# Kernel tuning notes

Hardware: AMD Instinct MI355X
Metric: run time of the kernel (lower is better)

The kernel has to match this reference:

```python
import jax, jax.numpy as jnp
import numpy as np

MIN_NORM = 1e-7

def _norm(x):
    return jnp.maximum(jnp.sqrt(jnp.sum(x * x, axis=-1, keepdims=True)), MIN_NORM)

def _artanh(x):
    return jnp.arctanh(jnp.clip(x, -1.0 + 1e-6, 1.0 - 1e-6))

def tan_k(x, k):
    sq = jnp.sqrt(-k)
    return jnp.tanh(sq * x) / sq

def artan_k(x, k):
    sq = jnp.sqrt(-k)
    return _artanh(sq * x) / sq

def mobius_add(x, y, k):
    xy = jnp.sum(x * y, axis=-1, keepdims=True)
    x2 = jnp.sum(x * x, axis=-1, keepdims=True)
    y2 = jnp.sum(y * y, axis=-1, keepdims=True)
    num = (1.0 - 2.0 * k * xy - k * y2) * x + (1.0 + k * x2) * y
    den = 1.0 - 2.0 * k * xy + (k * k) * x2 * y2
    return num / jnp.maximum(den, MIN_NORM)

def expmap0(u, k):
    un = _norm(u)
    return tan_k(un, k) * u / un

def logmap0(y, k):
    yn = _norm(y)
    return artan_k(yn, k) * y / yn

def mobius_matvec(M, x, k):
    mx = x @ M.T
    xn = _norm(x)
    mxn = _norm(mx)
    return tan_k(mxn / xn * artan_k(xn, k), k) * mx / mxn

def mobius_pmul(w, x, k):
    wx = w * x
    xn = _norm(x)
    wxn = _norm(wx)
    return tan_k(wxn / xn * artan_k(xn, k), k) * wx / wxn

def setup_inputs() -> dict:
    B, S, D_IN, H = 64, 128, 768, 768
    key = jax.random.key(0)
    ks = jax.random.split(key, 5)
    stdv = 1.0 / np.sqrt(H)
    # inputs scaled small so points lie well inside the Poincare ball
    inputs = jax.random.normal(ks[0], (B, S, D_IN), dtype=jnp.float32) * 1e-3
    timestamps = jax.random.uniform(ks[1], (B, S), dtype=jnp.float32)
    h0 = jnp.zeros((B, H), dtype=jnp.float32)
    c0 = jnp.zeros((B, H), dtype=jnp.float32)
    W_all = jax.random.uniform(ks[2], (H, 4 * H), minval=-stdv, maxval=stdv, dtype=jnp.float32)
    U_all = jax.random.uniform(ks[3], (4 * H, D_IN), minval=-stdv, maxval=stdv, dtype=jnp.float32)
    W_d = jax.random.uniform(ks[4], (H, H), minval=-stdv, maxval=stdv, dtype=jnp.float32)
    c = jnp.float32(-1.0)  # Poincare ball curvature
    return {"inputs": inputs, "timestamps": timestamps, "h0": h0, "c0": c0,
            "W_all": W_all, "U_all": U_all, "W_d": W_d, "c": c}

def reference(inputs, timestamps, h0, c0, W_all, U_all, W_d, c):
    k = c
    W_f, W_i, W_o, W_ct = jnp.split(W_all, 4, axis=1)
    U_f, U_i, U_o, U_ct = jnp.split(U_all, 4, axis=0)

    def one_rnn_transform(W, h, U, x):
        return mobius_add(mobius_matvec(W, h, k), mobius_matvec(U, x, k), k)

    def step(carry, xs):
        h, cc = carry
        x, t = xs  # x: (B, D_in), t: (B,)
        c_s1 = expmap0(jnp.tanh(logmap0(mobius_matvec(W_d, cc, k), k)), k)
        t_exp = jnp.broadcast_to(t[:, None], c_s1.shape)
        c_s2 = mobius_pmul(c_s1, t_exp, k)
        c_l = mobius_add(-c_s1, cc, k)
        c_adj = mobius_add(c_l, c_s2, k)
        f = jax.nn.sigmoid(logmap0(one_rnn_transform(W_f, h, U_f, x), k))
        i = jax.nn.sigmoid(logmap0(one_rnn_transform(W_i, h, U_i, x), k))
        o = jax.nn.sigmoid(logmap0(one_rnn_transform(W_o, h, U_o, x), k))
        c_tmp = jax.nn.sigmoid(logmap0(one_rnn_transform(W_ct, h, U_ct, x), k))
        new_c = mobius_add(mobius_pmul(i, c_tmp, k), mobius_pmul(f, c_adj, k), k)
        new_h = mobius_pmul(o, expmap0(jnp.tanh(new_c), k), k)
        return (new_h, new_c), o

    xs = (inputs.transpose(1, 0, 2), timestamps.T)  # seq-major for scan
    (h_last, c_last), outs = jax.lax.scan(step, (h0, c0), xs)
    outputs = outs.transpose(1, 0, 2)  # (B, S, H)
    return (outputs, h_last, c_last)
```

## Files before the change

kernel.cpp:

```cpp
#include <hip/hip_runtime.h>
#include <hip/hip_bf16.h>
#include <math.h>

#define MINN 1e-7f

#define BB 64
#define SS 128
#define NCOL 3840

typedef float f4 __attribute__((ext_vector_type(4)));
typedef short bf16x8 __attribute__((ext_vector_type(8)));
typedef float f32x4 __attribute__((ext_vector_type(4)));

__device__ __forceinline__ float artanh_c(float x) {
  x = fminf(fmaxf(x, -1.0f + 1e-6f), 1.0f - 1e-6f);
  return atanhf(x);
}
__device__ __forceinline__ float tan_k_(float x, float sq) { return tanhf(sq * x) / sq; }
__device__ __forceinline__ float artan_k_(float x, float sq) { return artanh_c(sq * x) / sq; }

template <int N>
__device__ __forceinline__ void block_reduce_sum(float* v, float* red) {
#pragma unroll
  for (int m = 1; m < 64; m <<= 1) {
#pragma unroll
    for (int i = 0; i < N; ++i) v[i] += __shfl_xor(v[i], m, 64);
  }
  int wid = threadIdx.x >> 6;
  int lane = threadIdx.x & 63;
  if (lane == 0) {
#pragma unroll
    for (int i = 0; i < N; ++i) red[wid * N + i] = v[i];
  }
  __syncthreads();
#pragma unroll
  for (int i = 0; i < N; ++i) v[i] = red[i] + red[N + i] + red[2 * N + i] + red[3 * N + i];
  __syncthreads();
}

__global__ __launch_bounds__(256) void k_build_cw(const float* __restrict__ W_all,
                                                  const float* __restrict__ W_d,
                                                  __hip_bfloat16* __restrict__ CWh,
                                                  __hip_bfloat16* __restrict__ CWl) {
  int col = blockIdx.x;
#pragma unroll
  for (int p = 0; p < 3; ++p) {
    int k = threadIdx.x + 256 * p;
    float v;
    if (col < 768) {
      v = W_d[col * 768 + k];
    } else {
      int jm = col - 768;
      int g = jm / 768;
      int j2 = jm - g * 768;
      v = W_all[j2 * 3072 + g * 768 + k];
    }
    __hip_bfloat16 h = __float2bfloat16(v);
    CWh[(size_t)col * 768 + k] = h;
    CWl[(size_t)col * 768 + k] = __float2bfloat16(v - __bfloat162float(h));
  }
}

__global__ __launch_bounds__(256) void k_init_state(
    const float* __restrict__ h0, const float* __restrict__ c0,
    float* __restrict__ ccR, float* __restrict__ hR,
    __hip_bfloat16* __restrict__ CH, __hip_bfloat16* __restrict__ CL,
    __hip_bfloat16* __restrict__ HH, __hip_bfloat16* __restrict__ HL) {
  int r = blockIdx.x;
#pragma unroll
  for (int p = 0; p < 3; ++p) {
    int j = threadIdx.x + 256 * p;
    float cv = c0[r * 768 + j];
    float hv = h0[r * 768 + j];
    ccR[r * 768 + j] = cv;
    hR[r * 768 + j] = hv;
    __hip_bfloat16 ch = __float2bfloat16(cv);
    CH[r * 768 + j] = ch;
    CL[r * 768 + j] = __float2bfloat16(cv - __bfloat162float(ch));
    __hip_bfloat16 hh = __float2bfloat16(hv);
    HH[r * 768 + j] = hh;
    HL[r * 768 + j] = __float2bfloat16(hv - __bfloat162float(hh));
  }
}

__global__ __launch_bounds__(256) void k_xnorm(const float* __restrict__ X,
                                               float* __restrict__ XN) {
  __shared__ float red[4];
  int r = blockIdx.x;
  float s = 0.f;
#pragma unroll
  for (int p = 0; p < 3; ++p) {
    float v = X[(size_t)r * 768 + threadIdx.x + 256 * p];
    s += v * v;
  }
#pragma unroll
  for (int m = 1; m < 64; m <<= 1) s += __shfl_xor(s, m, 64);
  if ((threadIdx.x & 63) == 0) red[threadIdx.x >> 6] = s;
  __syncthreads();
  if (threadIdx.x == 0) XN[r] = fmaxf(sqrtf(red[0] + red[1] + red[2] + red[3]), MINN);
}

__global__ __launch_bounds__(256) void k_split(const float* __restrict__ src,
                                               __hip_bfloat16* __restrict__ hi,
                                               __hip_bfloat16* __restrict__ lo, int n4) {
  int i = blockIdx.x * 256 + threadIdx.x;
  if (i >= n4) return;
  f4 v = *(const f4*)(src + (size_t)i * 4);
#pragma unroll
  for (int j = 0; j < 4; ++j) {
    float x = (j == 0) ? v.x : (j == 1) ? v.y : (j == 2) ? v.z : v.w;
    __hip_bfloat16 h = __float2bfloat16(x);
    float r = x - __bfloat162float(h);
    hi[(size_t)i * 4 + j] = h;
    lo[(size_t)i * 4 + j] = __float2bfloat16(r);
  }
}

__global__ __launch_bounds__(256) void k_gemm_xu_mfma(
    const __hip_bfloat16* __restrict__ Xh, const __hip_bfloat16* __restrict__ Xl,
    const __hip_bfloat16* __restrict__ Uh, const __hip_bfloat16* __restrict__ Ul,
    __hip_bfloat16* __restrict__ OUT) {
  int tid = threadIdx.x;
  int wave = tid >> 6, lane = tid & 63;
  int r = lane & 15, kg = lane >> 4;
  int i0 = blockIdx.x * 64 + wave * 16;
  int m0 = blockIdx.y * 64;
  const __hip_bfloat16* xh = Xh + (size_t)(i0 + r) * 768 + kg * 8;
  const __hip_bfloat16* xl = Xl + (size_t)(i0 + r) * 768 + kg * 8;
  const __hip_bfloat16* uh = Uh + (size_t)(m0 + r) * 768 + kg * 8;
  const __hip_bfloat16* ul = Ul + (size_t)(m0 + r) * 768 + kg * 8;
  f32x4 acc0 = {0.f, 0.f, 0.f, 0.f};
  f32x4 acc1 = acc0, acc2 = acc0, acc3 = acc0;
  for (int k0 = 0; k0 < 768; k0 += 32) {
    bf16x8 ah = *(const bf16x8*)(xh + k0);
    bf16x8 al = *(const bf16x8*)(xl + k0);
    bf16x8 b0h = *(const bf16x8*)(uh + k0);
    bf16x8 b0l = *(const bf16x8*)(ul + k0);
    bf16x8 b1h = *(const bf16x8*)(uh + 12288 + k0);
    bf16x8 b1l = *(const bf16x8*)(ul + 12288 + k0);
    bf16x8 b2h = *(const bf16x8*)(uh + 24576 + k0);
    bf16x8 b2l = *(const bf16x8*)(ul + 24576 + k0);
    bf16x8 b3h = *(const bf16x8*)(uh + 36864 + k0);
    bf16x8 b3l = *(const bf16x8*)(ul + 36864 + k0);
    acc0 = __builtin_amdgcn_mfma_f32_16x16x32_bf16(ah, b0h, acc0, 0, 0, 0);
    acc1 = __builtin_amdgcn_mfma_f32_16x16x32_bf16(ah, b1h, acc1, 0, 0, 0);
    acc2 = __builtin_amdgcn_mfma_f32_16x16x32_bf16(ah, b2h, acc2, 0, 0, 0);
    acc3 = __builtin_amdgcn_mfma_f32_16x16x32_bf16(ah, b3h, acc3, 0, 0, 0);
    acc0 = __builtin_amdgcn_mfma_f32_16x16x32_bf16(al, b0h, acc0, 0, 0, 0);
    acc1 = __builtin_amdgcn_mfma_f32_16x16x32_bf16(al, b1h, acc1, 0, 0, 0);
    acc2 = __builtin_amdgcn_mfma_f32_16x16x32_bf16(al, b2h, acc2, 0, 0, 0);
    acc3 = __builtin_amdgcn_mfma_f32_16x16x32_bf16(al, b3h, acc3, 0, 0, 0);
    acc0 = __builtin_amdgcn_mfma_f32_16x16x32_bf16(ah, b0l, acc0, 0, 0, 0);
    acc1 = __builtin_amdgcn_mfma_f32_16x16x32_bf16(ah, b1l, acc1, 0, 0, 0);
    acc2 = __builtin_amdgcn_mfma_f32_16x16x32_bf16(ah, b2l, acc2, 0, 0, 0);
    acc3 = __builtin_amdgcn_mfma_f32_16x16x32_bf16(ah, b3l, acc3, 0, 0, 0);
  }
#pragma unroll
  for (int j = 0; j < 4; ++j) {
    size_t row = (size_t)(i0 + kg * 4 + j) * 3072 + m0 + r;
    OUT[row] = __float2bfloat16(acc0[j]);
    OUT[row + 16] = __float2bfloat16(acc1[j]);
    OUT[row + 32] = __float2bfloat16(acc2[j]);
    OUT[row + 48] = __float2bfloat16(acc3[j]);
  }
}

__global__ __launch_bounds__(256) void k_step_gemm_mfma(
    const __hip_bfloat16* __restrict__ CWh, const __hip_bfloat16* __restrict__ CWl,
    const __hip_bfloat16* __restrict__ CH, const __hip_bfloat16* __restrict__ CL,
    const __hip_bfloat16* __restrict__ HH, const __hip_bfloat16* __restrict__ HL,
    float* __restrict__ GOUT) {
  int j = blockIdx.x;
  int wave = threadIdx.x >> 6, lane = threadIdx.x & 63;
  int r = lane & 15, kg = lane >> 4;
  int i0 = wave * 16;
  int m0 = j * 16;
  const __hip_bfloat16* sh = (j < 48 ? CH : HH) + (size_t)(i0 + r) * 768 + kg * 8;
  const __hip_bfloat16* sl = (j < 48 ? CL : HL) + (size_t)(i0 + r) * 768 + kg * 8;
  const __hip_bfloat16* wh = CWh + (size_t)(m0 + r) * 768 + kg * 8;
  const __hip_bfloat16* wl = CWl + (size_t)(m0 + r) * 768 + kg * 8;
  f32x4 acc = {0.f, 0.f, 0.f, 0.f};
#pragma unroll 4
  for (int k0 = 0; k0 < 768; k0 += 32) {
    bf16x8 ah = *(const bf16x8*)(sh + k0);
    bf16x8 al = *(const bf16x8*)(sl + k0);
    bf16x8 bh = *(const bf16x8*)(wh + k0);
    bf16x8 bl = *(const bf16x8*)(wl + k0);
    acc = __builtin_amdgcn_mfma_f32_16x16x32_bf16(ah, bh, acc, 0, 0, 0);
    acc = __builtin_amdgcn_mfma_f32_16x16x32_bf16(al, bh, acc, 0, 0, 0);
    acc = __builtin_amdgcn_mfma_f32_16x16x32_bf16(ah, bl, acc, 0, 0, 0);
  }
#pragma unroll
  for (int jj = 0; jj < 4; ++jj)
    GOUT[(size_t)(i0 + kg * 4 + jj) * NCOL + m0 + r] = acc[jj];
}

__global__ __launch_bounds__(256) void k_step_pw(
    const float* __restrict__ GOUT, const __hip_bfloat16* __restrict__ UG,
    const float* __restrict__ XN, const float* __restrict__ TS,
    const float* __restrict__ kptr, float* __restrict__ ccR, float* __restrict__ hR,
    __hip_bfloat16* __restrict__ CH, __hip_bfloat16* __restrict__ CL,
    __hip_bfloat16* __restrict__ HH, __hip_bfloat16* __restrict__ HL,
    float* __restrict__ out, int t) {
  __shared__ float red[64];
  int r = blockIdx.x;
  int tid = threadIdx.x;
  float kk = kptr[0];
  float sq = sqrtf(-kk);
  const float* grow = GOUT + r * NCOL;
  int i = r * SS + t;
  const __hip_bfloat16* urow = UG + (size_t)i * 3072;

  float cc[3], h[3], mv[3], gh[4][3], mx[4][3];
#pragma unroll
  for (int p = 0; p < 3; ++p) {
    int j = tid + 256 * p;
    cc[p] = ccR[r * 768 + j];
    h[p] = hR[r * 768 + j];
    mv[p] = grow[j];
#pragma unroll
    for (int g = 0; g < 4; ++g) {
      gh[g][p] = grow[768 + g * 768 + j];
      mx[g][p] = __bfloat162float(urow[g * 768 + j]);
    }
  }

  float sv[15];
#pragma unroll
  for (int q = 0; q < 15; ++q) sv[q] = 0.f;
#pragma unroll
  for (int p = 0; p < 3; ++p) {
    sv[0] += cc[p] * cc[p];
    sv[1] += h[p] * h[p];
    sv[2] += mv[p] * mv[p];
#pragma unroll
    for (int g = 0; g < 4; ++g) {
      sv[3 + g] += gh[g][p] * gh[g][p];
      sv[7 + g] += gh[g][p] * mx[g][p];
      sv[11 + g] += mx[g][p] * mx[g][p];
    }
  }
  block_reduce_sum<15>(sv, red);
  float c2 = sv[0], h2 = sv[1], mvn2 = sv[2];
  float xn_c = fmaxf(sqrtf(c2), MINN);
  float xn_h = fmaxf(sqrtf(h2), MINN);
  float mxn_d = fmaxf(sqrtf(mvn2), MINN);

  float r_d = (mxn_d / xn_c) * artan_k_(xn_c, sq);
  float twd = tan_k_(r_d, sq);
  float wdsc = twd / mxn_d;
  float yn_d = fmaxf(fabsf(twd), MINN);
  float lsc = (artan_k_(yn_d, sq) / yn_d) * wdsc;
  float th[3];
#pragma unroll
  for (int p = 0; p < 3; ++p) th[p] = tanhf(lsc * mv[p]);

  float uxn = XN[i];
  float ak_h = artan_k_(xn_h, sq);
  float ak_u = artan_k_(uxn, sq);
  float cAg[4], cBg[4], pscg[4];
#pragma unroll
  for (int g = 0; g < 4; ++g) {
    float ghn = fmaxf(sqrtf(sv[3 + g]), MINN);
    float tg = tan_k_((ghn / xn_h) * ak_h, sq);
    float wsc = tg / ghn;
    float w2 = tg * tg;
    float umxn = fmaxf(sqrtf(sv[11 + g]), MINN);
    float us = tan_k_((umxn / uxn) * ak_u, sq) / umxn;
    float u2 = us * us * sv[11 + g];
    float xy = wsc * us * sv[7 + g];
    float den = fmaxf(1.f - 2.f * kk * xy + kk * kk * w2 * u2, MINN);
    float a = (1.f - 2.f * kk * xy - kk * u2) / den;
    float b = (1.f + kk * w2) / den;
    float y2s = fmaxf(a * a * w2 + 2.f * a * b * xy + b * b * u2, 0.f);
    float yn = fmaxf(sqrtf(y2s), MINN);
    pscg[g] = artan_k_(yn, sq) / yn;
    cAg[g] = a * wsc;
    cBg[g] = b * us;
  }
  float gate[4][3];
#pragma unroll
  for (int g = 0; g < 4; ++g)
#pragma unroll
    for (int p = 0; p < 3; ++p)
      gate[g][p] = 1.f / (1.f + expf(-pscg[g] * (cAg[g] * gh[g][p] + cBg[g] * mx[g][p])));

  float s2v[2] = {0.f, 0.f};
#pragma unroll
  for (int p = 0; p < 3; ++p) {
    s2v[0] += th[p] * th[p];
    s2v[1] += th[p] * cc[p];
  }
  block_reduce_sum<2>(s2v, red);
  float un = fmaxf(sqrtf(s2v[0]), MINN);
  float esc = tan_k_(un, sq) / un;
  float cs1[3];
#pragma unroll
  for (int p = 0; p < 3; ++p) cs1[p] = esc * th[p];
  float d1 = esc * s2v[1];
  float s1sq = esc * esc * s2v[0];

  float tv = TS[r * SS + t];
  float xnt = fmaxf(sqrtf(768.f * tv * tv), MINN);
  float wxn_t = fmaxf(fabsf(tv) * sqrtf(s1sq), MINN);
  float s2s = tan_k_((wxn_t / xnt) * artan_k_(xnt, sq), sq) / wxn_t * tv;
  float s2sq = s2s * s2s * s1sq;

  float den_l = fmaxf(1.f + 2.f * kk * d1 + kk * kk * s1sq * c2, MINN);
  float al = (1.f + 2.f * kk * d1 - kk * c2) / den_l;
  float bl = (1.f + kk * s1sq) / den_l;
  float pcl = -al, qcl = bl;

  float xy2 = s2s * (pcl * s1sq + qcl * d1);
  float x2b = fmaxf(pcl * pcl * s1sq + 2.f * pcl * qcl * d1 + qcl * qcl * c2, 0.f);
  float y2b = s2sq;
  float den2 = fmaxf(1.f - 2.f * kk * xy2 + kk * kk * x2b * y2b, MINN);
  float a2 = (1.f - 2.f * kk * xy2 - kk * y2b) / den2;
  float b2 = (1.f + kk * x2b) / den2;
  float g1c = a2 * pcl + b2 * s2s;
  float g2c = a2 * qcl;
  float cadj[3];
#pragma unroll
  for (int p = 0; p < 3; ++p) cadj[p] = g1c * cs1[p] + g2c * cc[p];
  float adjsq = fmaxf(g1c * g1c * s1sq + 2.f * g1c * g2c * d1 + g2c * g2c * c2, 0.f);

  float wxi[3], wxf[3];
#pragma unroll
  for (int p = 0; p < 3; ++p) {
    wxi[p] = gate[1][p] * gate[3][p];
    wxf[p] = gate[0][p] * cadj[p];
  }
  float s3v[4] = {0.f, 0.f, 0.f, 0.f};
#pragma unroll
  for (int p = 0; p < 3; ++p) {
    s3v[0] += gate[3][p] * gate[3][p];
    s3v[1] += wxi[p] * wxi[p];
    s3v[2] += wxf[p] * wxf[p];
    s3v[3] += wxi[p] * wxf[p];
  }
  block_reduce_sum<4>(s3v, red);
  float xnct = fmaxf(sqrtf(s3v[0]), MINN);
  float wxni = fmaxf(sqrtf(s3v[1]), MINN);
  float psi = tan_k_((wxni / xnct) * artan_k_(xnct, sq), sq) / wxni;
  float pi2 = psi * psi * s3v[1];
  float xnadj = fmaxf(sqrtf(adjsq), MINN);
  float wxnf = fmaxf(sqrtf(s3v[2]), MINN);
  float psf = tan_k_((wxnf / xnadj) * artan_k_(xnadj, sq), sq) / wxnf;
  float pf2 = psf * psf * s3v[2];
  float xyp = psi * psf * s3v[3];
  float den3 = fmaxf(1.f - 2.f * kk * xyp + kk * kk * pi2 * pf2, MINN);
  float a3 = (1.f - 2.f * kk * xyp - kk * pf2) / den3;
  float b3 = (1.f + kk * pi2) / den3;
  float nc[3], tc[3];
#pragma unroll
  for (int p = 0; p < 3; ++p) {
    nc[p] = a3 * psi * wxi[p] + b3 * psf * wxf[p];
    tc[p] = tanhf(nc[p]);
  }
  float s4v[1] = {0.f};
#pragma unroll
  for (int p = 0; p < 3; ++p) s4v[0] += tc[p] * tc[p];
  block_reduce_sum<1>(s4v, red);
  float unh = fmaxf(sqrtf(s4v[0]), MINN);
  float ehs = tan_k_(unh, sq) / unh;
  float Esq = ehs * ehs * s4v[0];
  float En = fmaxf(sqrtf(Esq), MINN);
  float wxo[3];
#pragma unroll
  for (int p = 0; p < 3; ++p) wxo[p] = gate[2][p] * (ehs * tc[p]);
  float s5v[1] = {0.f};
#pragma unroll
  for (int p = 0; p < 3; ++p) s5v[0] += wxo[p] * wxo[p];
  block_reduce_sum<1>(s5v, red);
  float wxno = fmaxf(sqrtf(s5v[0]), MINN);
  float pso = tan_k_((wxno / En) * artan_k_(En, sq), sq) / wxno;

  size_t BSHc = (size_t)BB * SS * 768;
#pragma unroll
  for (int p = 0; p < 3; ++p) {
    int j = tid + 256 * p;
    out[((size_t)r * SS + t) * 768 + j] = gate[2][p];
    float ncv = nc[p];
    float nhv = pso * wxo[p];
    ccR[r * 768 + j] = ncv;
    hR[r * 768 + j] = nhv;
    __hip_bfloat16 chh = __float2bfloat16(ncv);
    CH[r * 768 + j] = chh;
    CL[r * 768 + j] = __float2bfloat16(ncv - __bfloat162float(chh));
    __hip_bfloat16 hhh = __float2bfloat16(nhv);
    HH[r * 768 + j] = hhh;
    HL[r * 768 + j] = __float2bfloat16(nhv - __bfloat162float(hhh));
    if (t == SS - 1) {
      out[BSHc + (size_t)r * 768 + j] = nhv;
      out[BSHc + (size_t)BB * 768 + (size_t)r * 768 + j] = ncv;
    }
  }
}

extern "C" void kernel_launch(void* const* d_in, const int* in_sizes, int n_in,
                              void* d_out, int out_size, void* d_ws, size_t ws_size,
                              hipStream_t stream) {
  const float* inputs = (const float*)d_in[0];
  const float* ts = (const float*)d_in[1];
  const float* h0 = (const float*)d_in[2];
  const float* c0 = (const float*)d_in[3];
  const float* W_all = (const float*)d_in[4];
  const float* U_all = (const float*)d_in[5];
  const float* W_d = (const float*)d_in[6];
  const float* kptr = (const float*)d_in[7];
  float* ws = (float*)d_ws;
  float* out = (float*)d_out;

  size_t oCWH = 0;
  size_t oCWL = oCWH + 1474560;
  size_t oCCR = oCWL + 1474560;
  size_t oHR = oCCR + 49152;
  size_t oCH = oHR + 49152;
  size_t oCL = oCH + 24576;
  size_t oHH = oCL + 24576;
  size_t oHL = oHH + 24576;
  size_t oGOUT = oHL + 24576;
  size_t oXN = oGOUT + (size_t)BB * NCOL;
  size_t oUG = oXN + 8192;
  size_t oXH = oUG + 12582912;
  size_t oXL = oXH + 3145728;
  size_t oUH = oXL + 3145728;
  size_t oUL = oUH + 1179648;

  __hip_bfloat16* cwh = (__hip_bfloat16*)(ws + oCWH);
  __hip_bfloat16* cwl = (__hip_bfloat16*)(ws + oCWL);
  float* ccr = ws + oCCR;
  float* hr = ws + oHR;
  __hip_bfloat16* ch = (__hip_bfloat16*)(ws + oCH);
  __hip_bfloat16* cl = (__hip_bfloat16*)(ws + oCL);
  __hip_bfloat16* hh = (__hip_bfloat16*)(ws + oHH);
  __hip_bfloat16* hl = (__hip_bfloat16*)(ws + oHL);
  float* gout = ws + oGOUT;
  float* xn = ws + oXN;
  __hip_bfloat16* ug = (__hip_bfloat16*)(ws + oUG);
  __hip_bfloat16* xhh = (__hip_bfloat16*)(ws + oXH);
  __hip_bfloat16* xll = (__hip_bfloat16*)(ws + oXL);
  __hip_bfloat16* uhh = (__hip_bfloat16*)(ws + oUH);
  __hip_bfloat16* ull = (__hip_bfloat16*)(ws + oUL);

  k_build_cw<<<NCOL, 256, 0, stream>>>(W_all, W_d, cwh, cwl);
  k_init_state<<<BB, 256, 0, stream>>>(h0, c0, ccr, hr, ch, cl, hh, hl);
  k_split<<<(6291456 / 4 + 255) / 256, 256, 0, stream>>>(inputs, xhh, xll, 6291456 / 4);
  k_split<<<(2359296 / 4 + 255) / 256, 256, 0, stream>>>(U_all, uhh, ull, 2359296 / 4);
  k_gemm_xu_mfma<<<dim3(128, 48), 256, 0, stream>>>(xhh, xll, uhh, ull, ug);
  k_xnorm<<<BB * SS, 256, 0, stream>>>(inputs, xn);

  for (int t = 0; t < SS; ++t) {
    k_step_gemm_mfma<<<240, 256, 0, stream>>>(cwh, cwl, ch, cl, hh, hl, gout);
    k_step_pw<<<BB, 256, 0, stream>>>(gout, ug, xn, ts, kptr, ccr, hr, ch, cl, hh, hl,
                                      out, t);
  }
}
```

Measured before the change: 4.203 ms.

## Fuse per-step GEMM and pointwise kernels using an atomic-counter grid barrier

Merges the recurrent GEMM kernel and the pointwise update kernel into a single launch per timestep. All 240 blocks compute their GEMM tile and increment a global counter. The first 64 blocks then spin until the counter reaches the target for this step and run the pointwise phase. This removes one kernel launch and its inter-kernel gap per step. In exchange it relies on all blocks being co-resident, and on volatile accesses without explicit fences for memory visibility.

```diff
diff --git a/kernel.cpp b/kernel.cpp
--- a/kernel.cpp
+++ b/kernel.cpp
@@ -165,46 +165,56 @@
   }
 }
 
-__global__ __launch_bounds__(256) void k_step_gemm_mfma(
+__global__ __launch_bounds__(256) void k_step(
     const __hip_bfloat16* __restrict__ CWh, const __hip_bfloat16* __restrict__ CWl,
-    const __hip_bfloat16* __restrict__ CH, const __hip_bfloat16* __restrict__ CL,
-    const __hip_bfloat16* __restrict__ HH, const __hip_bfloat16* __restrict__ HL,
-    float* __restrict__ GOUT) {
-  int j = blockIdx.x;
-  int wave = threadIdx.x >> 6, lane = threadIdx.x & 63;
-  int r = lane & 15, kg = lane >> 4;
-  int i0 = wave * 16;
-  int m0 = j * 16;
-  const __hip_bfloat16* sh = (j < 48 ? CH : HH) + (size_t)(i0 + r) * 768 + kg * 8;
-  const __hip_bfloat16* sl = (j < 48 ? CL : HL) + (size_t)(i0 + r) * 768 + kg * 8;
-  const __hip_bfloat16* wh = CWh + (size_t)(m0 + r) * 768 + kg * 8;
-  const __hip_bfloat16* wl = CWl + (size_t)(m0 + r) * 768 + kg * 8;
-  f32x4 acc = {0.f, 0.f, 0.f, 0.f};
-#pragma unroll 4
-  for (int k0 = 0; k0 < 768; k0 += 32) {
-    bf16x8 ah = *(const bf16x8*)(sh + k0);
-    bf16x8 al = *(const bf16x8*)(sl + k0);
-    bf16x8 bh = *(const bf16x8*)(wh + k0);
-    bf16x8 bl = *(const bf16x8*)(wl + k0);
-    acc = __builtin_amdgcn_mfma_f32_16x16x32_bf16(ah, bh, acc, 0, 0, 0);
-    acc = __builtin_amdgcn_mfma_f32_16x16x32_bf16(al, bh, acc, 0, 0, 0);
-    acc = __builtin_amdgcn_mfma_f32_16x16x32_bf16(ah, bl, acc, 0, 0, 0);
-  }
-#pragma unroll
-  for (int jj = 0; jj < 4; ++jj)
-    GOUT[(size_t)(i0 + kg * 4 + jj) * NCOL + m0 + r] = acc[jj];
-}
-
-__global__ __launch_bounds__(256) void k_step_pw(
-    const float* __restrict__ GOUT, const __hip_bfloat16* __restrict__ UG,
-    const float* __restrict__ XN, const float* __restrict__ TS,
-    const float* __restrict__ kptr, float* __restrict__ ccR, float* __restrict__ hR,
+    float* __restrict__ GOUT, unsigned int* __restrict__ cnt,
+    const __hip_bfloat16* __restrict__ UG, const float* __restrict__ XN,
+    const float* __restrict__ TS, const float* __restrict__ kptr,
+    float* __restrict__ ccR, float* __restrict__ hR,
     __hip_bfloat16* __restrict__ CH, __hip_bfloat16* __restrict__ CL,
     __hip_bfloat16* __restrict__ HH, __hip_bfloat16* __restrict__ HL,
     float* __restrict__ out, int t) {
   __shared__ float red[64];
-  int r = blockIdx.x;
+  int j = blockIdx.x;
   int tid = threadIdx.x;
+
+  {
+    int wave = tid >> 6, lane = tid & 63;
+    int r = lane & 15, kg = lane >> 4;
+    int i0 = wave * 16;
+    int m0 = j * 16;
+    const __hip_bfloat16* sh = (j < 48 ? CH : HH) + (size_t)(i0 + r) * 768 + kg * 8;
+    const __hip_bfloat16* sl = (j < 48 ? CL : HL) + (size_t)(i0 + r) * 768 + kg * 8;
+    const __hip_bfloat16* wh = CWh + (size_t)(m0 + r) * 768 + kg * 8;
+    const __hip_bfloat16* wl = CWl + (size_t)(m0 + r) * 768 + kg * 8;
+    f32x4 acc = {0.f, 0.f, 0.f, 0.f};
+#pragma unroll 4
+    for (int k0 = 0; k0 < 768; k0 += 32) {
+      bf16x8 ah = *(const bf16x8*)(sh + k0);
+      bf16x8 al = *(const bf16x8*)(sl + k0);
+      bf16x8 bh = *(const bf16x8*)(wh + k0);
+      bf16x8 bl = *(const bf16x8*)(wl + k0);
+      acc = __builtin_amdgcn_mfma_f32_16x16x32_bf16(ah, bh, acc, 0, 0, 0);
+      acc = __builtin_amdgcn_mfma_f32_16x16x32_bf16(al, bh, acc, 0, 0, 0);
+      acc = __builtin_amdgcn_mfma_f32_16x16x32_bf16(ah, bl, acc, 0, 0, 0);
+    }
+#pragma unroll
+    for (int jj = 0; jj < 4; ++jj)
+      *(volatile float*)&GOUT[(size_t)(i0 + kg * 4 + jj) * NCOL + m0 + r] = acc[jj];
+  }
+  __syncthreads();
+  if (tid == 0) atomicAdd(cnt, 1u);
+  if (j >= BB) return;
+
+  unsigned int target = 240u * (unsigned int)(t + 1);
+  if (tid == 0) {
+    while (__hip_atomic_load(cnt, __ATOMIC_RELAXED, __HIP_MEMORY_SCOPE_AGENT) < target) {
+      __builtin_amdgcn_s_sleep(4);
+    }
+  }
+  __syncthreads();
+
+  int r = j;
   float kk = kptr[0];
   float sq = sqrtf(-kk);
   const float* grow = GOUT + r * NCOL;
@@ -214,14 +224,14 @@
   float cc[3], h[3], mv[3], gh[4][3], mx[4][3];
 #pragma unroll
   for (int p = 0; p < 3; ++p) {
-    int j = tid + 256 * p;
-    cc[p] = ccR[r * 768 + j];
-    h[p] = hR[r * 768 + j];
-    mv[p] = grow[j];
+    int jj = tid + 256 * p;
+    cc[p] = ccR[r * 768 + jj];
+    h[p] = hR[r * 768 + jj];
+    mv[p] = *(volatile const float*)&grow[jj];
 #pragma unroll
     for (int g = 0; g < 4; ++g) {
-      gh[g][p] = grow[768 + g * 768 + j];
-      mx[g][p] = __bfloat162float(urow[g * 768 + j]);
+      gh[g][p] = *(volatile const float*)&grow[768 + g * 768 + jj];
+      mx[g][p] = __bfloat162float(urow[g * 768 + jj]);
     }
   }
 
@@ -378,21 +388,21 @@
   size_t BSHc = (size_t)BB * SS * 768;
 #pragma unroll
   for (int p = 0; p < 3; ++p) {
-    int j = tid + 256 * p;
-    out[((size_t)r * SS + t) * 768 + j] = gate[2][p];
+    int jj = tid + 256 * p;
+    out[((size_t)r * SS + t) * 768 + jj] = gate[2][p];
     float ncv = nc[p];
     float nhv = pso * wxo[p];
-    ccR[r * 768 + j] = ncv;
-    hR[r * 768 + j] = nhv;
+    ccR[r * 768 + jj] = ncv;
+    hR[r * 768 + jj] = nhv;
     __hip_bfloat16 chh = __float2bfloat16(ncv);
-    CH[r * 768 + j] = chh;
-    CL[r * 768 + j] = __float2bfloat16(ncv - __bfloat162float(chh));
+    CH[r * 768 + jj] = chh;
+    CL[r * 768 + jj] = __float2bfloat16(ncv - __bfloat162float(chh));
     __hip_bfloat16 hhh = __float2bfloat16(nhv);
-    HH[r * 768 + j] = hhh;
-    HL[r * 768 + j] = __float2bfloat16(nhv - __bfloat162float(hhh));
+    HH[r * 768 + jj] = hhh;
+    HL[r * 768 + jj] = __float2bfloat16(nhv - __bfloat162float(hhh));
     if (t == SS - 1) {
-      out[BSHc + (size_t)r * 768 + j] = nhv;
-      out[BSHc + (size_t)BB * 768 + (size_t)r * 768 + j] = ncv;
+      out[BSHc + (size_t)r * 768 + jj] = nhv;
+      out[BSHc + (size_t)BB * 768 + (size_t)r * 768 + jj] = ncv;
     }
   }
 }
@@ -411,7 +421,8 @@
   float* ws = (float*)d_ws;
   float* out = (float*)d_out;
 
-  size_t oCWH = 0;
+  size_t oCNT = 0;
+  size_t oCWH = 16;
   size_t oCWL = oCWH + 1474560;
   size_t oCCR = oCWL + 1474560;
   size_t oHR = oCCR + 49152;
@@ -427,6 +438,7 @@
   size_t oUH = oXL + 3145728;
   size_t oUL = oUH + 1179648;
 
+  unsigned int* cnt = (unsigned int*)(ws + oCNT);
   __hip_bfloat16* cwh = (__hip_bfloat16*)(ws + oCWH);
   __hip_bfloat16* cwl = (__hip_bfloat16*)(ws + oCWL);
   float* ccr = ws + oCCR;
@@ -443,6 +455,7 @@
   __hip_bfloat16* uhh = (__hip_bfloat16*)(ws + oUH);
   __hip_bfloat16* ull = (__hip_bfloat16*)(ws + oUL);
 
+  hipMemsetAsync(cnt, 0, 64, stream);
   k_build_cw<<<NCOL, 256, 0, stream>>>(W_all, W_d, cwh, cwl);
   k_init_state<<<BB, 256, 0, stream>>>(h0, c0, ccr, hr, ch, cl, hh, hl);
   k_split<<<(6291456 / 4 + 255) / 256, 256, 0, stream>>>(inputs, xhh, xll, 6291456 / 4);
@@ -451,8 +464,7 @@
   k_xnorm<<<BB * SS, 256, 0, stream>>>(inputs, xn);
 
   for (int t = 0; t < SS; ++t) {
-    k_step_gemm_mfma<<<240, 256, 0, stream>>>(cwh, cwl, ch, cl, hh, hl, gout);
-    k_step_pw<<<BB, 256, 0, stream>>>(gout, ug, xn, ts, kptr, ccr, hr, ch, cl, hh, hl,
-                                      out, t);
-  }
-}
+    k_step<<<240, 256, 0, stream>>>(cwh, cwl, gout, cnt, ug, xn, ts, kptr, ccr, hr,
+                                    ch, cl, hh, hl, out, t);
+  }
+}
```

New measurement: 5.081 ms. 1.21x slower.

## Split-K recurrent GEMM, retile input GEMM, merge final pointwise reductions

Applied to the files above, without the earlier changes.

The per-step recurrent GEMM now has each block compute 64 output columns (four 16-column tiles) over half of K, giving 120 blocks. Each K half writes its own partial buffer, and the pointwise kernel sums the two halves. The input-projection GEMM now computes 32 rows per wave and drops the U low-part correction term, which reduces loads and MFMAs at some cost in precision. In the pointwise kernel, the norm of o*tanh(c) is folded into the same block reduction as tanh(c), which removes one block-wide reduction and barrier per step.

```diff
diff --git a/kernel.cpp b/kernel.cpp
--- a/kernel.cpp
+++ b/kernel.cpp
@@ -118,85 +118,90 @@
 
 __global__ __launch_bounds__(256) void k_gemm_xu_mfma(
     const __hip_bfloat16* __restrict__ Xh, const __hip_bfloat16* __restrict__ Xl,
-    const __hip_bfloat16* __restrict__ Uh, const __hip_bfloat16* __restrict__ Ul,
-    __hip_bfloat16* __restrict__ OUT) {
+    const __hip_bfloat16* __restrict__ Uh, __hip_bfloat16* __restrict__ OUT) {
   int tid = threadIdx.x;
   int wave = tid >> 6, lane = tid & 63;
   int r = lane & 15, kg = lane >> 4;
-  int i0 = blockIdx.x * 64 + wave * 16;
+  int i0 = blockIdx.x * 128 + wave * 32;
   int m0 = blockIdx.y * 64;
-  const __hip_bfloat16* xh = Xh + (size_t)(i0 + r) * 768 + kg * 8;
-  const __hip_bfloat16* xl = Xl + (size_t)(i0 + r) * 768 + kg * 8;
+  const __hip_bfloat16* xh0 = Xh + (size_t)(i0 + r) * 768 + kg * 8;
+  const __hip_bfloat16* xh1 = Xh + (size_t)(i0 + 16 + r) * 768 + kg * 8;
+  const __hip_bfloat16* xl0 = Xl + (size_t)(i0 + r) * 768 + kg * 8;
+  const __hip_bfloat16* xl1 = Xl + (size_t)(i0 + 16 + r) * 768 + kg * 8;
   const __hip_bfloat16* uh = Uh + (size_t)(m0 + r) * 768 + kg * 8;
-  const __hip_bfloat16* ul = Ul + (size_t)(m0 + r) * 768 + kg * 8;
-  f32x4 acc0 = {0.f, 0.f, 0.f, 0.f};
-  f32x4 acc1 = acc0, acc2 = acc0, acc3 = acc0;
+  f32x4 acc[2][4];
+#pragma unroll
+  for (int a = 0; a < 2; ++a)
+#pragma unroll
+    for (int b = 0; b < 4; ++b) acc[a][b] = {0.f, 0.f, 0.f, 0.f};
   for (int k0 = 0; k0 < 768; k0 += 32) {
-    bf16x8 ah = *(const bf16x8*)(xh + k0);
-    bf16x8 al = *(const bf16x8*)(xl + k0);
-    bf16x8 b0h = *(const bf16x8*)(uh + k0);
-    bf16x8 b0l = *(const bf16x8*)(ul + k0);
-    bf16x8 b1h = *(const bf16x8*)(uh + 12288 + k0);
-    bf16x8 b1l = *(const bf16x8*)(ul + 12288 + k0);
-    bf16x8 b2h = *(const bf16x8*)(uh + 24576 + k0);
-    bf16x8 b2l = *(const bf16x8*)(ul + 24576 + k0);
-    bf16x8 b3h = *(const bf16x8*)(uh + 36864 + k0);
-    bf16x8 b3l = *(const bf16x8*)(ul + 36864 + k0);
-    acc0 = __builtin_amdgcn_mfma_f32_16x16x32_bf16(ah, b0h, acc0, 0, 0, 0);
-    acc1 = __builtin_amdgcn_mfma_f32_16x16x32_bf16(ah, b1h, acc1, 0, 0, 0);
-    acc2 = __builtin_amdgcn_mfma_f32_16x16x32_bf16(ah, b2h, acc2, 0, 0, 0);
-    acc3 = __builtin_amdgcn_mfma_f32_16x16x32_bf16(ah, b3h, acc3, 0, 0, 0);
-    acc0 = __builtin_amdgcn_mfma_f32_16x16x32_bf16(al, b0h, acc0, 0, 0, 0);
-    acc1 = __builtin_amdgcn_mfma_f32_16x16x32_bf16(al, b1h, acc1, 0, 0, 0);
-    acc2 = __builtin_amdgcn_mfma_f32_16x16x32_bf16(al, b2h, acc2, 0, 0, 0);
-    acc3 = __builtin_amdgcn_mfma_f32_16x16x32_bf16(al, b3h, acc3, 0, 0, 0);
-    acc0 = __builtin_amdgcn_mfma_f32_16x16x32_bf16(ah, b0l, acc0, 0, 0, 0);
-    acc1 = __builtin_amdgcn_mfma_f32_16x16x32_bf16(ah, b1l, acc1, 0, 0, 0);
-    acc2 = __builtin_amdgcn_mfma_f32_16x16x32_bf16(ah, b2l, acc2, 0, 0, 0);
-    acc3 = __builtin_amdgcn_mfma_f32_16x16x32_bf16(ah, b3l, acc3, 0, 0, 0);
-  }
-#pragma unroll
-  for (int j = 0; j < 4; ++j) {
-    size_t row = (size_t)(i0 + kg * 4 + j) * 3072 + m0 + r;
-    OUT[row] = __float2bfloat16(acc0[j]);
-    OUT[row + 16] = __float2bfloat16(acc1[j]);
-    OUT[row + 32] = __float2bfloat16(acc2[j]);
-    OUT[row + 48] = __float2bfloat16(acc3[j]);
-  }
+    bf16x8 ah0 = *(const bf16x8*)(xh0 + k0);
+    bf16x8 ah1 = *(const bf16x8*)(xh1 + k0);
+    bf16x8 al0 = *(const bf16x8*)(xl0 + k0);
+    bf16x8 al1 = *(const bf16x8*)(xl1 + k0);
+    bf16x8 bh[4];
+#pragma unroll
+    for (int p = 0; p < 4; ++p) bh[p] = *(const bf16x8*)(uh + p * 12288 + k0);
+#pragma unroll
+    for (int p = 0; p < 4; ++p) {
+      acc[0][p] = __builtin_amdgcn_mfma_f32_16x16x32_bf16(ah0, bh[p], acc[0][p], 0, 0, 0);
+      acc[1][p] = __builtin_amdgcn_mfma_f32_16x16x32_bf16(ah1, bh[p], acc[1][p], 0, 0, 0);
+      acc[0][p] = __builtin_amdgcn_mfma_f32_16x16x32_bf16(al0, bh[p], acc[0][p], 0, 0, 0);
+      acc[1][p] = __builtin_amdgcn_mfma_f32_16x16x32_bf16(al1, bh[p], acc[1][p], 0, 0, 0);
+    }
+  }
+#pragma unroll
+  for (int a = 0; a < 2; ++a)
+#pragma unroll
+    for (int p = 0; p < 4; ++p)
+#pragma unroll
+      for (int jj = 0; jj < 4; ++jj)
+        OUT[(size_t)(i0 + a * 16 + kg * 4 + jj) * 3072 + m0 + p * 16 + r] =
+            __float2bfloat16(acc[a][p][jj]);
 }
 
 __global__ __launch_bounds__(256) void k_step_gemm_mfma(
     const __hip_bfloat16* __restrict__ CWh, const __hip_bfloat16* __restrict__ CWl,
     const __hip_bfloat16* __restrict__ CH, const __hip_bfloat16* __restrict__ CL,
     const __hip_bfloat16* __restrict__ HH, const __hip_bfloat16* __restrict__ HL,
-    float* __restrict__ GOUT) {
-  int j = blockIdx.x;
+    float* __restrict__ GOUT2) {
+  int cg = blockIdx.x;
+  int kh = blockIdx.y;
   int wave = threadIdx.x >> 6, lane = threadIdx.x & 63;
   int r = lane & 15, kg = lane >> 4;
   int i0 = wave * 16;
-  int m0 = j * 16;
-  const __hip_bfloat16* sh = (j < 48 ? CH : HH) + (size_t)(i0 + r) * 768 + kg * 8;
-  const __hip_bfloat16* sl = (j < 48 ? CL : HL) + (size_t)(i0 + r) * 768 + kg * 8;
-  const __hip_bfloat16* wh = CWh + (size_t)(m0 + r) * 768 + kg * 8;
-  const __hip_bfloat16* wl = CWl + (size_t)(m0 + r) * 768 + kg * 8;
-  f32x4 acc = {0.f, 0.f, 0.f, 0.f};
+  int m0 = cg * 64;
+  int kb = kh * 384;
+  const __hip_bfloat16* sh = (cg < 12 ? CH : HH) + (size_t)(i0 + r) * 768 + kb + kg * 8;
+  const __hip_bfloat16* sl = (cg < 12 ? CL : HL) + (size_t)(i0 + r) * 768 + kb + kg * 8;
+  const __hip_bfloat16* wh = CWh + (size_t)(m0 + r) * 768 + kb + kg * 8;
+  const __hip_bfloat16* wl = CWl + (size_t)(m0 + r) * 768 + kb + kg * 8;
+  f32x4 acc[4];
+#pragma unroll
+  for (int p = 0; p < 4; ++p) acc[p] = {0.f, 0.f, 0.f, 0.f};
 #pragma unroll 4
-  for (int k0 = 0; k0 < 768; k0 += 32) {
+  for (int k0 = 0; k0 < 384; k0 += 32) {
     bf16x8 ah = *(const bf16x8*)(sh + k0);
     bf16x8 al = *(const bf16x8*)(sl + k0);
-    bf16x8 bh = *(const bf16x8*)(wh + k0);
-    bf16x8 bl = *(const bf16x8*)(wl + k0);
-    acc = __builtin_amdgcn_mfma_f32_16x16x32_bf16(ah, bh, acc, 0, 0, 0);
-    acc = __builtin_amdgcn_mfma_f32_16x16x32_bf16(al, bh, acc, 0, 0, 0);
-    acc = __builtin_amdgcn_mfma_f32_16x16x32_bf16(ah, bl, acc, 0, 0, 0);
-  }
-#pragma unroll
-  for (int jj = 0; jj < 4; ++jj)
-    GOUT[(size_t)(i0 + kg * 4 + jj) * NCOL + m0 + r] = acc[jj];
+#pragma unroll
+    for (int p = 0; p < 4; ++p) {
+      bf16x8 bh = *(const bf16x8*)(wh + p * 12288 + k0);
+      bf16x8 bl = *(const bf16x8*)(wl + p * 12288 + k0);
+      acc[p] = __builtin_amdgcn_mfma_f32_16x16x32_bf16(ah, bh, acc[p], 0, 0, 0);
+      acc[p] = __builtin_amdgcn_mfma_f32_16x16x32_bf16(al, bh, acc[p], 0, 0, 0);
+      acc[p] = __builtin_amdgcn_mfma_f32_16x16x32_bf16(ah, bl, acc[p], 0, 0, 0);
+    }
+  }
+  float* gout = GOUT2 + (size_t)kh * (BB * NCOL);
+#pragma unroll
+  for (int p = 0; p < 4; ++p)
+#pragma unroll
+    for (int jj = 0; jj < 4; ++jj)
+      gout[(size_t)(i0 + kg * 4 + jj) * NCOL + m0 + p * 16 + r] = acc[p][jj];
 }
 
 __global__ __launch_bounds__(256) void k_step_pw(
-    const float* __restrict__ GOUT, const __hip_bfloat16* __restrict__ UG,
+    const float* __restrict__ GOUT2, const __hip_bfloat16* __restrict__ UG,
     const float* __restrict__ XN, const float* __restrict__ TS,
     const float* __restrict__ kptr, float* __restrict__ ccR, float* __restrict__ hR,
     __hip_bfloat16* __restrict__ CH, __hip_bfloat16* __restrict__ CL,
@@ -207,7 +212,8 @@
   int tid = threadIdx.x;
   float kk = kptr[0];
   float sq = sqrtf(-kk);
-  const float* grow = GOUT + r * NCOL;
+  const float* grow0 = GOUT2 + (size_t)r * NCOL;
+  const float* grow1 = GOUT2 + (size_t)BB * NCOL + (size_t)r * NCOL;
   int i = r * SS + t;
   const __hip_bfloat16* urow = UG + (size_t)i * 3072;
 
@@ -217,10 +223,10 @@
     int j = tid + 256 * p;
     cc[p] = ccR[r * 768 + j];
     h[p] = hR[r * 768 + j];
-    mv[p] = grow[j];
+    mv[p] = grow0[j] + grow1[j];
 #pragma unroll
     for (int g = 0; g < 4; ++g) {
-      gh[g][p] = grow[768 + g * 768 + j];
+      gh[g][p] = grow0[768 + g * 768 + j] + grow1[768 + g * 768 + j];
       mx[g][p] = __bfloat162float(urow[g * 768 + j]);
     }
   }
@@ -357,22 +363,19 @@
     nc[p] = a3 * psi * wxi[p] + b3 * psf * wxf[p];
     tc[p] = tanhf(nc[p]);
   }
-  float s4v[1] = {0.f};
-#pragma unroll
-  for (int p = 0; p < 3; ++p) s4v[0] += tc[p] * tc[p];
-  block_reduce_sum<1>(s4v, red);
+  float s4v[2] = {0.f, 0.f};
+#pragma unroll
+  for (int p = 0; p < 3; ++p) {
+    s4v[0] += tc[p] * tc[p];
+    float gt = gate[2][p] * tc[p];
+    s4v[1] += gt * gt;
+  }
+  block_reduce_sum<2>(s4v, red);
   float unh = fmaxf(sqrtf(s4v[0]), MINN);
   float ehs = tan_k_(unh, sq) / unh;
   float Esq = ehs * ehs * s4v[0];
   float En = fmaxf(sqrtf(Esq), MINN);
-  float wxo[3];
-#pragma unroll
-  for (int p = 0; p < 3; ++p) wxo[p] = gate[2][p] * (ehs * tc[p]);
-  float s5v[1] = {0.f};
-#pragma unroll
-  for (int p = 0; p < 3; ++p) s5v[0] += wxo[p] * wxo[p];
-  block_reduce_sum<1>(s5v, red);
-  float wxno = fmaxf(sqrtf(s5v[0]), MINN);
+  float wxno = fmaxf(ehs * sqrtf(s4v[1]), MINN);
   float pso = tan_k_((wxno / En) * artan_k_(En, sq), sq) / wxno;
 
   size_t BSHc = (size_t)BB * SS * 768;
@@ -381,7 +384,7 @@
     int j = tid + 256 * p;
     out[((size_t)r * SS + t) * 768 + j] = gate[2][p];
     float ncv = nc[p];
-    float nhv = pso * wxo[p];
+    float nhv = pso * (gate[2][p] * (ehs * tc[p]));
     ccR[r * 768 + j] = ncv;
     hR[r * 768 + j] = nhv;
     __hip_bfloat16 chh = __float2bfloat16(ncv);
@@ -420,7 +423,7 @@
   size_t oHH = oCL + 24576;
   size_t oHL = oHH + 24576;
   size_t oGOUT = oHL + 24576;
-  size_t oXN = oGOUT + (size_t)BB * NCOL;
+  size_t oXN = oGOUT + 2 * (size_t)BB * NCOL;
   size_t oUG = oXN + 8192;
   size_t oXH = oUG + 12582912;
   size_t oXL = oXH + 3145728;
@@ -447,11 +450,11 @@
   k_init_state<<<BB, 256, 0, stream>>>(h0, c0, ccr, hr, ch, cl, hh, hl);
   k_split<<<(6291456 / 4 + 255) / 256, 256, 0, stream>>>(inputs, xhh, xll, 6291456 / 4);
   k_split<<<(2359296 / 4 + 255) / 256, 256, 0, stream>>>(U_all, uhh, ull, 2359296 / 4);
-  k_gemm_xu_mfma<<<dim3(128, 48), 256, 0, stream>>>(xhh, xll, uhh, ull, ug);
+  k_gemm_xu_mfma<<<dim3(64, 48), 256, 0, stream>>>(xhh, xll, uhh, ug);
   k_xnorm<<<BB * SS, 256, 0, stream>>>(inputs, xn);
 
   for (int t = 0; t < SS; ++t) {
-    k_step_gemm_mfma<<<240, 256, 0, stream>>>(cwh, cwl, ch, cl, hh, hl, gout);
+    k_step_gemm_mfma<<<dim3(60, 2), 256, 0, stream>>>(cwh, cwl, ch, cl, hh, hl, gout);
     k_step_pw<<<BB, 256, 0, stream>>>(gout, ug, xn, ts, kptr, ccr, hr, ch, cl, hh, hl,
                                       out, t);
   }
```

After: 4.119 ms. 2.0% less time.
